# Performance work log

Measured on AMD Instinct MI355X. Metric: run time of the kernel, lower is better.

## Reference

```python
import jax, jax.numpy as jnp
import numpy as np
import math

LUT_RES = 512
TWO_PI = 2.0 * math.pi
# LUT tables: sin/cos sampled uniformly over [0, 2*pi)
_SIN_TABLE = jnp.sin(jnp.arange(LUT_RES, dtype=jnp.float32) * (TWO_PI / LUT_RES))


def _lut_idx(phase):
    # phase mod 2*pi mapped to [0, LUT_RES) integer bin (floor lookup)
    frac = jnp.mod(phase, TWO_PI) * (1.0 / TWO_PI)
    return (frac * LUT_RES).astype(jnp.int32) % LUT_RES


def setup_inputs() -> dict:
    key = jax.random.key(0)
    k1, k2, k3 = jax.random.split(key, 3)
    B, S, E, N = 2, 1024, 128, 512
    x = jax.random.normal(k1, (B, S, E), dtype=jnp.float32)
    w = jax.random.normal(k2, (E, N), dtype=jnp.float32) * 0.1          # init_freq_scale
    b = jax.random.uniform(k3, (E, N), dtype=jnp.float32) * TWO_PI      # init_offset_scale
    t = jnp.arange(S, dtype=jnp.float32)
    return {"x": x, "w": w, "b": b, "t": t}


def reference(x, w, b, t):
    # phase: (B, S, E, N) = w*x (broadcast outer product) + b + t
    phase = (w[None, None, :, :] * x[:, :, :, None]
             + b[None, None, :, :]
             + t[None, :, None, None])
    sin_vals = _SIN_TABLE[_lut_idx(phase)]   # LUT sin lookup
    return sin_vals.sum(axis=2)              # reduce over embed_dim -> (B, S, N)
```

## Files before the change

kernel.cpp:

```cpp
#include <hip/hip_runtime.h>
#include <math.h>


constexpr int E_DIM = 128;
constexpr int N_DIM = 512;
constexpr int ST    = 8;
constexpr int TPB   = 256;

__global__ __launch_bounds__(TPB) void sin_layer_kernel(
    const float* __restrict__ x,
    const float* __restrict__ w,
    const float* __restrict__ bv_,
    const float* __restrict__ t,
    float* __restrict__ out,
    int S)
{
    constexpr float SCALE  = 512.0f * 0.15915493667125702f;
    constexpr float INV512 = 1.0f / 512.0f;

    const int nh  = blockIdx.x & 1;
    const int g   = blockIdx.x >> 1;
    const int n   = nh * TPB + threadIdx.x;
    const int bs0 = g * ST;

    float tn[ST];
    float acc[ST];
    const float* xr[ST];
#pragma unroll
    for (int i = 0; i < ST; ++i) {
        const int bs = bs0 + i;
        const int s  = (bs >= S) ? (bs - S) : bs;
        tn[i]  = t[s] * SCALE;
        xr[i]  = x + (size_t)bs * E_DIM;
        acc[i] = 0.0f;
    }

    const float* wp = w   + n;
    const float* bp = bv_ + n;

#pragma unroll 4
    for (int e = 0; e < E_DIM; ++e) {
        const float wv = wp[(size_t)e * N_DIM];
        const float bv = bp[(size_t)e * N_DIM];
        const float wn = wv * SCALE;
        float btn[ST];
#pragma unroll
        for (int i = 0; i < ST; ++i)
            btn[i] = __fmaf_rn(bv, SCALE, tn[i]);
#pragma unroll
        for (int i = 0; i < ST; ++i) {
            const float xv = xr[i][e];
            float u = __fmaf_rn(wn, xv, btn[i]);
            float k = floorf(u);
            acc[i] += __builtin_amdgcn_sinf(k * INV512);
        }
    }

#pragma unroll
    for (int i = 0; i < ST; ++i) {
        out[(size_t)(bs0 + i) * N_DIM + n] = acc[i];
    }
}

extern "C" void kernel_launch(void* const* d_in, const int* in_sizes, int n_in,
                              void* d_out, int out_size, void* d_ws, size_t ws_size,
                              hipStream_t stream) {
    const float* x = (const float*)d_in[0];
    const float* w = (const float*)d_in[1];
    const float* b = (const float*)d_in[2];
    const float* t = (const float*)d_in[3];
    float* out = (float*)d_out;

    const int S  = in_sizes[3];
    const int BS = in_sizes[0] / E_DIM;

    const int grid = (BS / ST) * (N_DIM / TPB);
    sin_layer_kernel<<<grid, TPB, 0, stream>>>(x, w, b, t, out, S);
}
```

Baseline: 88.07 us.

## Split embedding reduction across blocks and add a separate partial-sum reduce kernel

Splits the 128-wide embedding loop into 4 chunks, each handled by its own block, which quadruples the grid. The goal is more waves per CU, so the latency of the sin and load instructions is better hidden than with the original 512-block launch. Partial sums go to workspace memory, and a second vectorised kernel adds the four partials into the output. The cost is an extra kernel launch plus writing and reading roughly 16 MB of partials.

```diff
diff --git a/kernel.cpp b/kernel.cpp
--- a/kernel.cpp
+++ b/kernel.cpp
@@ -6,22 +6,27 @@
 constexpr int N_DIM = 512;
 constexpr int ST    = 8;
 constexpr int TPB   = 256;
+constexpr int EC    = 4;
+constexpr int ECH   = E_DIM / EC;
 
-__global__ __launch_bounds__(TPB) void sin_layer_kernel(
+__global__ __launch_bounds__(TPB) void sin_layer_partial(
     const float* __restrict__ x,
     const float* __restrict__ w,
     const float* __restrict__ bv_,
     const float* __restrict__ t,
-    float* __restrict__ out,
-    int S)
+    float* __restrict__ part,
+    int S, int BS)
 {
     constexpr float SCALE  = 512.0f * 0.15915493667125702f;
     constexpr float INV512 = 1.0f / 512.0f;
 
-    const int nh  = blockIdx.x & 1;
-    const int g   = blockIdx.x >> 1;
+    const int bid = blockIdx.x;
+    const int ec  = bid & (EC - 1);
+    const int nh  = (bid >> 2) & 1;
+    const int g   = bid >> 3;
     const int n   = nh * TPB + threadIdx.x;
     const int bs0 = g * ST;
+    const int e0  = ec * ECH;
 
     float tn[ST];
     float acc[ST];
@@ -31,22 +36,22 @@
         const int bs = bs0 + i;
         const int s  = (bs >= S) ? (bs - S) : bs;
         tn[i]  = t[s] * SCALE;
-        xr[i]  = x + (size_t)bs * E_DIM;
+        xr[i]  = x + (size_t)bs * E_DIM + e0;
         acc[i] = 0.0f;
     }
 
-    const float* wp = w   + n;
-    const float* bp = bv_ + n;
+    const float* wp = w   + (size_t)e0 * N_DIM + n;
+    const float* bp = bv_ + (size_t)e0 * N_DIM + n;
 
 #pragma unroll 4
-    for (int e = 0; e < E_DIM; ++e) {
+    for (int e = 0; e < ECH; ++e) {
         const float wv = wp[(size_t)e * N_DIM];
-        const float bv = bp[(size_t)e * N_DIM];
+        const float bb = bp[(size_t)e * N_DIM];
         const float wn = wv * SCALE;
         float btn[ST];
 #pragma unroll
         for (int i = 0; i < ST; ++i)
-            btn[i] = __fmaf_rn(bv, SCALE, tn[i]);
+            btn[i] = __fmaf_rn(bb, SCALE, tn[i]);
 #pragma unroll
         for (int i = 0; i < ST; ++i) {
             const float xv = xr[i][e];
@@ -56,10 +61,31 @@
         }
     }
 
+    float* pp = part + (size_t)ec * BS * N_DIM;
 #pragma unroll
     for (int i = 0; i < ST; ++i) {
-        out[(size_t)(bs0 + i) * N_DIM + n] = acc[i];
+        pp[(size_t)(bs0 + i) * N_DIM + n] = acc[i];
     }
+}
+
+__global__ __launch_bounds__(TPB) void sin_layer_reduce(
+    const float* __restrict__ part,
+    float* __restrict__ out,
+    int nvec)
+{
+    const int i = blockIdx.x * TPB + threadIdx.x;
+    if (i >= nvec) return;
+    const float4* p = (const float4*)part;
+    float4 a = p[i];
+    float4 b = p[i + (size_t)nvec];
+    float4 c = p[i + (size_t)2 * nvec];
+    float4 d = p[i + (size_t)3 * nvec];
+    float4 o;
+    o.x = (a.x + b.x) + (c.x + d.x);
+    o.y = (a.y + b.y) + (c.y + d.y);
+    o.z = (a.z + b.z) + (c.z + d.z);
+    o.w = (a.w + b.w) + (c.w + d.w);
+    ((float4*)out)[i] = o;
 }
 
 extern "C" void kernel_launch(void* const* d_in, const int* in_sizes, int n_in,
@@ -69,11 +95,16 @@
     const float* w = (const float*)d_in[1];
     const float* b = (const float*)d_in[2];
     const float* t = (const float*)d_in[3];
-    float* out = (float*)d_out;
+    float* out  = (float*)d_out;
+    float* part = (float*)d_ws;
 
     const int S  = in_sizes[3];
     const int BS = in_sizes[0] / E_DIM;
 
-    const int grid = (BS / ST) * (N_DIM / TPB);
-    sin_layer_kernel<<<grid, TPB, 0, stream>>>(x, w, b, t, out, S);
+    const int grid1 = (BS / ST) * 2 * EC;
+    sin_layer_partial<<<grid1, TPB, 0, stream>>>(x, w, b, t, part, S, BS);
+
+    const int nvec  = out_size / 4;
+    const int grid2 = (nvec + TPB - 1) / TPB;
+    sin_layer_reduce<<<grid2, TPB, 0, stream>>>(part, out, nvec);
 }
```

Measured after the change: 92.35 us. 4.9% more time.
